# Optimization experiments

Hardware: AMD Instinct MI355X
Metric: run time of the kernel (lower is better)

Reference implementation:

```python
import jax, jax.numpy as jnp
import numpy as np
from jax import lax

GROUPS = 32


def _fps(xyz, m):
    # farthest point sampling; indices are non-differentiable selections
    xyz = lax.stop_gradient(xyz)
    B, N, _ = xyz.shape

    def step(carry, _):
        dist, far = carry
        c = jnp.take_along_axis(xyz, far[:, None, None], axis=1)  # [B,1,3]
        d = jnp.sum((xyz - c) ** 2, axis=-1)                       # [B,N]
        dist = jnp.minimum(dist, d)
        return (dist, jnp.argmax(dist, axis=1)), far

    init = (jnp.full((B, N), 1e10, xyz.dtype), jnp.zeros((B,), jnp.int32))
    _, cent = lax.scan(step, init, None, length=m)
    return jnp.transpose(cent)  # [B,m]


def _sqdist(a, b):
    # [B,Na,3] x [B,Nb,3] -> [B,Na,Nb]
    return (jnp.sum(a * a, -1)[:, :, None] + jnp.sum(b * b, -1)[:, None, :]
            - 2.0 * jnp.einsum('bnc,bmc->bnm', a, b))


def _gather(feat, idx):
    # feat [B,S,C], idx [B,N,k] -> [B,N,k,C]
    return jax.vmap(lambda f, i: f[i])(feat, idx)


def _edge_conv(f, idx, W, b):
    nbr = _gather(f, idx)                                # [B,S,k,C]
    ctr = jnp.broadcast_to(f[:, :, None, :], nbr.shape)
    e = jnp.concatenate([ctr, nbr - ctr], axis=-1)       # [B,S,k,2C]
    h = jax.nn.relu(jnp.einsum('bske,ec->bskc', e, W) + b)
    return jnp.max(h, axis=2)                            # [B,S,C']


def _graph_encoder(x, k, layers, Wo, bo):
    d2 = _sqdist(x[..., :3], x[..., :3])
    idx = lax.top_k(-d2, k)[1]                           # kNN on coords (incl. self)
    f = x
    for W, b in layers:
        f = _edge_conv(f, idx, W, b)
    return f @ Wo + bo


def _upsample(fs, xd, xs):
    # 3-NN inverse-distance interpolation, matches torch.cdist/topk path
    d = jnp.sqrt(jnp.maximum(_sqdist(xd, xs), 0.0))      # euclidean like cdist
    negv, idx = lax.top_k(-d, 3)
    w = 1.0 / (-negv + 1e-8)
    w = w / jnp.sum(w, -1, keepdims=True)
    fk = _gather(fs, idx)                                # [B,Nd,3,C]
    return jnp.sum(fk * w[..., None], axis=2)


def _group_norm(x, g, b):
    B, N, C = x.shape
    xg = x.reshape(B, N, GROUPS, C // GROUPS)
    mu = xg.mean(-1, keepdims=True)
    var = xg.var(-1, keepdims=True)
    xn = ((xg - mu) * lax.rsqrt(var + 1e-5)).reshape(B, N, C)
    return xn * g + b


def _pos_encoding(N, d):
    pos = jnp.arange(N, dtype=jnp.float32)[:, None]
    div = jnp.exp(jnp.arange(0, d, 2, dtype=jnp.float32) * (-np.log(10000.0) / d))
    ang = pos * div
    return jnp.stack([jnp.sin(ang), jnp.cos(ang)], axis=-1).reshape(N, d)


def _forward(x,
             e1_W0, e1_b0, e1_W1, e1_b1, e1_Wo, e1_bo,
             e2_W0, e2_b0, e2_W1, e2_b1, e2_Wo, e2_bo,
             e3_W0, e3_b0, e3_W1, e3_b1, e3_W2, e3_b2, e3_Wo, e3_bo,
             f_W1, f_b1, g1_w, g1_b, f_W2, f_b2, g2_w, g2_b):
    B, N, C = x.shape
    encs = [
        (512, 16, [(e1_W0, e1_b0), (e1_W1, e1_b1)], e1_Wo, e1_bo),
        (1024, 32, [(e2_W0, e2_b0), (e2_W1, e2_b1)], e2_Wo, e2_bo),
        (2048, 64, [(e3_W0, e3_b0), (e3_W1, e3_b1), (e3_W2, e3_b2)], e3_Wo, e3_bo),
    ]
    feats = []
    for scale, k, layers, Wo, bo in encs:
        if N > scale:
            idx = _fps(x[..., :3], scale)
            xs = jnp.take_along_axis(x, idx[:, :, None], axis=1)  # [B,scale,C]
        else:
            xs = x
        f = _graph_encoder(xs, k, layers, Wo, bo)
        if f.shape[1] < N:
            f = _upsample(f, x[..., :3], xs[..., :3])
        feats.append(f)
    fused = jnp.concatenate(feats, axis=-1)               # [B,N,1280]
    h = jax.nn.relu(_group_norm(fused @ f_W1 + f_b1, g1_w, g1_b))
    h = jax.nn.relu(_group_norm(h @ f_W2 + f_b2, g2_w, g2_b))
    return h + _pos_encoding(N, h.shape[-1])[None]


def setup_inputs() -> dict:
    key = jax.random.key(0)
    ks = iter(jax.random.split(key, 64))

    def W(shape, s=0.05):
        return jax.random.normal(next(ks), shape, jnp.float32) * s

    inp = {"x": jax.random.normal(next(ks), (2, 4096, 6), jnp.float32)}
    # encoder 1: in 6, hidden [128,256], out 256, k=16
    inp.update(e1_W0=W((12, 128)), e1_b0=jnp.zeros(128), e1_W1=W((256, 256)), e1_b1=jnp.zeros(256),
               e1_Wo=W((256, 256)), e1_bo=jnp.zeros(256))
    # encoder 2: in 6, hidden [256,512], out 512, k=32
    inp.update(e2_W0=W((12, 256)), e2_b0=jnp.zeros(256), e2_W1=W((512, 512)), e2_b1=jnp.zeros(512),
               e2_Wo=W((512, 512)), e2_bo=jnp.zeros(512))
    # encoder 3: in 6, hidden [128,256,512], out 512, k=64
    inp.update(e3_W0=W((12, 128)), e3_b0=jnp.zeros(128), e3_W1=W((256, 256)), e3_b1=jnp.zeros(256),
               e3_W2=W((512, 512)), e3_b2=jnp.zeros(512), e3_Wo=W((512, 512)), e3_bo=jnp.zeros(512))
    # fusion: 1280 -> 512 -> 512 with GroupNorm(32, 512)
    inp.update(f_W1=W((1280, 512)), f_b1=jnp.zeros(512), g1_w=jnp.ones(512), g1_b=jnp.zeros(512),
               f_W2=W((512, 512)), f_b2=jnp.zeros(512), g2_w=jnp.ones(512), g2_b=jnp.zeros(512))
    return inp


def reference(x,
              e1_W0, e1_b0, e1_W1, e1_b1, e1_Wo, e1_bo,
              e2_W0, e2_b0, e2_W1, e2_b1, e2_Wo, e2_bo,
              e3_W0, e3_b0, e3_W1, e3_b1, e3_W2, e3_b2, e3_Wo, e3_bo,
              f_W1, f_b1, g1_w, g1_b, f_W2, f_b2, g2_w, g2_b):
    return _forward(x,
                    e1_W0, e1_b0, e1_W1, e1_b1, e1_Wo, e1_bo,
                    e2_W0, e2_b0, e2_W1, e2_b1, e2_Wo, e2_bo,
                    e3_W0, e3_b0, e3_W1, e3_b1, e3_W2, e3_b2, e3_Wo, e3_bo,
                    f_W1, f_b1, g1_w, g1_b, f_W2, f_b2, g2_w, g2_b)
```

## Files before the change

### kernel.cpp

```cpp
#include <hip/hip_runtime.h>
#include <math.h>

#define OFF_CENT   0x0
#define OFF_XSP    0x20000
#define OFF_XS6    0x40000
#define OFF_KNN    0x60000
#define OFF_F      0x180000
#define OFF_UV     0xA00000
#define OFF_G      0x1A00000
#define OFF_WCAT   0x2200000
#define OFF_BCAT   0x2400000
#define OFF_FUSED  0x2500000
#define OFF_T      0x180000
#define OFF_H1     0x1200000
#define OFF_T2     0x2200000

__device__ __forceinline__ unsigned fkey_flip(float f) {
  unsigned u = __float_as_uint(f);
  return u ^ ((u >> 31) ? 0xFFFFFFFFu : 0x80000000u);
}
__device__ __forceinline__ float fkey_unflip(unsigned k) {
  unsigned u = k ^ ((k >> 31) ? 0x80000000u : 0xFFFFFFFFu);
  return __uint_as_float(u);
}

template<int CTRL>
__device__ __forceinline__ float dpp_max_stepf(float v) {
  int t = __builtin_amdgcn_update_dpp(__float_as_int(v), __float_as_int(v),
                                      CTRL, 0xf, 0xf, false);
  return fmaxf(v, __int_as_float(t));
}
__device__ __forceinline__ float wave64_max(float v) {
  v = dpp_max_stepf<0x111>(v);
  v = dpp_max_stepf<0x112>(v);
  v = dpp_max_stepf<0x114>(v);
  v = dpp_max_stepf<0x118>(v);
  v = dpp_max_stepf<0x142>(v);
  v = dpp_max_stepf<0x143>(v);
  return __int_as_float(__builtin_amdgcn_readlane(__float_as_int(v), 63));
}
__device__ __forceinline__ unsigned long long u64max(unsigned long long a,
                                                    unsigned long long b) {
  return a > b ? a : b;
}

__global__ __launch_bounds__(512) void fps_kernel(const float* __restrict__ x,
                                                  int* __restrict__ cent)
{
  int b = blockIdx.x, tid = threadIdx.x;
  __shared__ float4 C4[4096];
  __shared__ __align__(16) unsigned long long slots[2][8];
  float px[8], py[8], pz[8], dist[8];
#pragma unroll
  for (int i = 0; i < 8; ++i) {
    int p = tid + 512 * i;
    const float* r = x + ((long)b * 4096 + p) * 6;
    px[i] = r[0]; py[i] = r[1]; pz[i] = r[2];
    C4[p] = make_float4(px[i], py[i], pz[i], 0.0f);
    dist[i] = 1e10f;
  }
  if (tid == 0) cent[b * 2048] = 0;
  __syncthreads();
  float4 c0 = C4[0];
  float cx = c0.x, cy = c0.y, cz = c0.z;
  int wid = tid >> 6, lane = tid & 63;
  for (int j = 1; j < 2048; ++j) {
    float m = -1.0f;
#pragma unroll
    for (int i = 0; i < 8; ++i) {
      float dx = __fsub_rn(px[i], cx);
      float dy = __fsub_rn(py[i], cy);
      float dz = __fsub_rn(pz[i], cz);
      float d  = __fadd_rn(__fadd_rn(__fmul_rn(dx,dx), __fmul_rn(dy,dy)), __fmul_rn(dz,dz));
      float nd = fminf(dist[i], d);
      dist[i] = nd;
      m = fmaxf(m, nd);
    }
    float wm = wave64_max(m);
    unsigned long long mm = 0ULL; unsigned ii = 0;
#pragma unroll
    for (int i = 7; i >= 0; --i) {
      unsigned long long mi = __ballot(dist[i] == wm);
      if (mi) { mm = mi; ii = (unsigned)i; }
    }
    int lane_w = __ffsll((unsigned long long)mm) - 1;
    unsigned idx_w = (unsigned)(wid * 64 + lane_w) + 512u * ii;
    if (lane == 0)
      slots[j & 1][wid] = ((unsigned long long)__float_as_uint(wm) << 32)
                        | (unsigned)(0xFFFFFFFFu - idx_w);
    __syncthreads();
    const unsigned long long* sl = slots[j & 1];
    ulonglong2 sA = *(const ulonglong2*)&sl[0];
    ulonglong2 sB = *(const ulonglong2*)&sl[2];
    ulonglong2 sC = *(const ulonglong2*)&sl[4];
    ulonglong2 sD = *(const ulonglong2*)&sl[6];
    unsigned long long kk = u64max(u64max(u64max(sA.x, sA.y), u64max(sB.x, sB.y)),
                                   u64max(u64max(sC.x, sC.y), u64max(sD.x, sD.y)));
    unsigned idx = 0xFFFFFFFFu - (unsigned)kk;
    float4 c = C4[idx];
    cx = c.x; cy = c.y; cz = c.z;
    if (tid == 0) cent[b * 2048 + j] = idx;
  }
}

__global__ void gather_xs_kernel(const float* __restrict__ x, const int* __restrict__ cent,
                                 float* __restrict__ xs6, float4* __restrict__ xsp)
{
  int t = blockIdx.x * 256 + threadIdx.x;
  if (t >= 2 * 2048) return;
  int b = t >> 11;
  int p = cent[t];
  const float* src = x + ((long)b * 4096 + p) * 6;
  float* dst = xs6 + (long)t * 6;
#pragma unroll
  for (int c = 0; c < 6; ++c) dst[c] = src[c];
  xsp[t] = make_float4(src[0], src[1], src[2], 0.0f);
}

template<int S, int K>
__global__ __launch_bounds__(256) void knn_kernel(const float4* __restrict__ xsp,
                                                  int* __restrict__ out)
{
  constexpr int NI = S / 64;
  __shared__ float4 P[S];
  int b = (blockIdx.x * 4) / S;
  int wid = threadIdx.x >> 6, lane = threadIdx.x & 63;
  int s = (blockIdx.x * 4 + wid) & (S - 1);
  for (int i = threadIdx.x; i < S; i += 256) P[i] = xsp[b * 2048 + i];
  __syncthreads();
  float4 Q = P[s];
  float saq = __fadd_rn(__fadd_rn(__fmul_rn(Q.x,Q.x), __fmul_rn(Q.y,Q.y)), __fmul_rn(Q.z,Q.z));
  float dd[NI];
#pragma unroll
  for (int i = 0; i < NI; ++i) {
    float4 c = P[i * 64 + lane];
    float sac = __fadd_rn(__fadd_rn(__fmul_rn(c.x,c.x), __fmul_rn(c.y,c.y)), __fmul_rn(c.z,c.z));
    float dot = __fadd_rn(__fadd_rn(__fmul_rn(Q.x,c.x), __fmul_rn(Q.y,c.y)), __fmul_rn(Q.z,c.z));
    dd[i] = __fsub_rn(__fadd_rn(saq, sac), __fmul_rn(2.0f, dot));
  }
  long obase = ((long)b * S + s) * K;
  for (int t = 0; t < K; ++t) {
    float bv = INFINITY; int bi = 0;
#pragma unroll
    for (int i = 0; i < NI; ++i) if (dd[i] < bv) { bv = dd[i]; bi = i; }
    unsigned long long key = ((unsigned long long)fkey_flip(bv) << 32)
                           | (unsigned)(bi * 64 + lane);
#pragma unroll
    for (int m = 32; m; m >>= 1) {
      unsigned long long o = __shfl_xor(key, m, 64);
      if (o < key) key = o;
    }
    unsigned cand = (unsigned)key;
    if ((int)(cand & 63) == lane) {
      int slot = cand >> 6;
#pragma unroll
      for (int i = 0; i < NI; ++i) if (i == slot) dd[i] = INFINITY;
    }
    if (lane == 0) out[obase + t] = (int)cand;
  }
}

__global__ void wcat_prep(const float* __restrict__ W, const float* __restrict__ bias,
                          int C, int Cp, float* __restrict__ Wcat, float* __restrict__ bcat)
{
  int n2 = 2 * Cp;
  int total = C * n2;
  for (int t = blockIdx.x * 256 + threadIdx.x; t < total + n2; t += gridDim.x * 256) {
    if (t < total) {
      int c = t / n2, n = t % n2;
      Wcat[t] = (n < Cp) ? (W[c * Cp + n] - W[(C + c) * Cp + n]) : W[(C + c) * Cp + (n - Cp)];
    } else {
      int n = t - total;
      bcat[n] = (n < Cp) ? bias[n] : 0.0f;
    }
  }
}

__global__ __launch_bounds__(256) void gemm_bias(
    const float* __restrict__ A, long strideA, int lda,
    const float* __restrict__ W, int N, int K,
    const float* __restrict__ bias,
    float* __restrict__ C, long strideC, int ldc)
{
  A += (long)blockIdx.z * strideA;
  C += (long)blockIdx.z * strideC;
  int rowBase = blockIdx.x * 64, colBase = blockIdx.y * 64;
  __shared__ float As[16][68];
  __shared__ float Ws[16][68];
  int tid = threadIdx.x;
  int tx = tid & 15, ty = tid >> 4;
  float acc[4][4] = {};
  for (int k0 = 0; k0 < K; k0 += 16) {
    {
      int r = tid >> 2, c0 = (tid & 3) * 4;
      const float* Ar = A + (long)(rowBase + r) * lda + k0 + c0;
#pragma unroll
      for (int u = 0; u < 4; ++u) {
        float val = 0.0f;
        if (k0 + c0 + u < K) val = Ar[u];
        As[c0 + u][r] = val;
      }
    }
    {
      int c = tid & 63, kr = tid >> 6;
#pragma unroll
      for (int u = 0; u < 4; ++u) {
        int kk = kr + u * 4;
        float val = 0.0f;
        if (k0 + kk < K) val = W[(long)(k0 + kk) * N + colBase + c];
        Ws[kk][c] = val;
      }
    }
    __syncthreads();
#pragma unroll
    for (int kk = 0; kk < 16; ++kk) {
      float4 av = *(const float4*)&As[kk][ty * 4];
      float4 wv = *(const float4*)&Ws[kk][tx * 4];
      float a_[4] = {av.x, av.y, av.z, av.w};
      float w_[4] = {wv.x, wv.y, wv.z, wv.w};
#pragma unroll
      for (int i = 0; i < 4; ++i)
#pragma unroll
        for (int j = 0; j < 4; ++j)
          acc[i][j] = fmaf(a_[i], w_[j], acc[i][j]);
    }
    __syncthreads();
  }
#pragma unroll
  for (int i = 0; i < 4; ++i) {
    int r = rowBase + ty * 4 + i;
    int c0 = colBase + tx * 4;
    float4 o;
    o.x = acc[i][0] + bias[c0 + 0];
    o.y = acc[i][1] + bias[c0 + 1];
    o.z = acc[i][2] + bias[c0 + 2];
    o.w = acc[i][3] + bias[c0 + 3];
    *(float4*)&C[(long)r * ldc + c0] = o;
  }
}

__global__ __launch_bounds__(256) void gemm_bias_big(
    const float* __restrict__ A, int lda,
    const float* __restrict__ W, int N, int K,
    const float* __restrict__ bias,
    float* __restrict__ C, int ldc)
{
  int rowBase = blockIdx.x * 128, colBase = blockIdx.y * 128;
  __shared__ float As[16][132];
  __shared__ float Ws[16][132];
  int tid = threadIdx.x;
  int tx = tid & 15, ty = tid >> 4;
  float acc[8][8] = {};
  for (int k0 = 0; k0 < K; k0 += 16) {
    {
      int r = tid >> 1, c0 = (tid & 1) * 8;
      const float* Ar = A + (long)(rowBase + r) * lda + k0 + c0;
      float4 v0 = *(const float4*)(Ar);
      float4 v1 = *(const float4*)(Ar + 4);
      As[c0 + 0][r] = v0.x; As[c0 + 1][r] = v0.y; As[c0 + 2][r] = v0.z; As[c0 + 3][r] = v0.w;
      As[c0 + 4][r] = v1.x; As[c0 + 5][r] = v1.y; As[c0 + 6][r] = v1.z; As[c0 + 7][r] = v1.w;
    }
    {
      int kr = tid >> 4, c0 = (tid & 15) * 8;
      const float* Wr = W + (long)(k0 + kr) * N + colBase + c0;
      float4 w0 = *(const float4*)(Wr);
      float4 w1 = *(const float4*)(Wr + 4);
      *(float4*)&Ws[kr][c0]     = w0;
      *(float4*)&Ws[kr][c0 + 4] = w1;
    }
    __syncthreads();
#pragma unroll
    for (int kk = 0; kk < 16; ++kk) {
      float a_[8], w_[8];
      *(float4*)&a_[0] = *(const float4*)&As[kk][ty * 8];
      *(float4*)&a_[4] = *(const float4*)&As[kk][ty * 8 + 4];
      *(float4*)&w_[0] = *(const float4*)&Ws[kk][tx * 8];
      *(float4*)&w_[4] = *(const float4*)&Ws[kk][tx * 8 + 4];
#pragma unroll
      for (int i = 0; i < 8; ++i)
#pragma unroll
        for (int jj = 0; jj < 8; ++jj)
          acc[i][jj] = fmaf(a_[i], w_[jj], acc[i][jj]);
    }
    __syncthreads();
  }
#pragma unroll
  for (int i = 0; i < 8; ++i) {
    int r = rowBase + ty * 8 + i;
    int c0 = colBase + tx * 8;
    float4 o0, o1;
    o0.x = acc[i][0] + bias[c0 + 0];
    o0.y = acc[i][1] + bias[c0 + 1];
    o0.z = acc[i][2] + bias[c0 + 2];
    o0.w = acc[i][3] + bias[c0 + 3];
    o1.x = acc[i][4] + bias[c0 + 4];
    o1.y = acc[i][5] + bias[c0 + 5];
    o1.z = acc[i][6] + bias[c0 + 6];
    o1.w = acc[i][7] + bias[c0 + 7];
    *(float4*)&C[(long)r * ldc + c0]     = o0;
    *(float4*)&C[(long)r * ldc + c0 + 4] = o1;
  }
}

__global__ void edge_agg(const float* __restrict__ UV, const int* __restrict__ idx,
                         int S, int k, int Cp, float* __restrict__ F)
{
  int bs = blockIdx.x;
  int b = bs / S;
  __shared__ int nb[64];
  if ((int)threadIdx.x < k) nb[threadIdx.x] = idx[(long)bs * k + threadIdx.x];
  __syncthreads();
  int ld = 2 * Cp;
  const float* Ub = UV + (long)bs * ld;
  for (int c = threadIdx.x; c < Cp; c += blockDim.x) {
    float m = -INFINITY;
    for (int j = 0; j < k; ++j) {
      float v = UV[(long)(b * S + nb[j]) * ld + Cp + c];
      m = fmaxf(m, v);
    }
    float r = Ub[c] + m;
    F[(long)bs * Cp + c] = r > 0.0f ? r : 0.0f;
  }
}

template<int S, int CP>
__global__ __launch_bounds__(256) void upsample_kernel(
    const float* __restrict__ x, const float4* __restrict__ xsp,
    const float* __restrict__ G, float* __restrict__ fused, int colOff)
{
  constexpr int NI = S / 64;
  __shared__ float4 P[S];
  int b = (blockIdx.x * 4) >> 12;
  int wid = threadIdx.x >> 6, lane = threadIdx.x & 63;
  int n = (blockIdx.x * 4 + wid) & 4095;
  for (int i = threadIdx.x; i < S; i += 256) P[i] = xsp[b * 2048 + i];
  __syncthreads();
  const float* q = x + ((long)b * 4096 + n) * 6;
  float qx = q[0], qy = q[1], qz = q[2];
  float saq = __fadd_rn(__fadd_rn(__fmul_rn(qx,qx), __fmul_rn(qy,qy)), __fmul_rn(qz,qz));
  float dd[NI];
#pragma unroll
  for (int i = 0; i < NI; ++i) {
    float4 c = P[i * 64 + lane];
    float sac = __fadd_rn(__fadd_rn(__fmul_rn(c.x,c.x), __fmul_rn(c.y,c.y)), __fmul_rn(c.z,c.z));
    float dot = __fadd_rn(__fadd_rn(__fmul_rn(qx,c.x), __fmul_rn(qy,c.y)), __fmul_rn(qz,c.z));
    dd[i] = __fsub_rn(__fadd_rn(saq, sac), __fmul_rn(2.0f, dot));
  }
  int id[3]; float w[3];
  for (int t = 0; t < 3; ++t) {
    float bv = INFINITY; int bi = 0;
#pragma unroll
    for (int i = 0; i < NI; ++i) if (dd[i] < bv) { bv = dd[i]; bi = i; }
    unsigned long long key = ((unsigned long long)fkey_flip(bv) << 32)
                           | (unsigned)(bi * 64 + lane);
#pragma unroll
    for (int m = 32; m; m >>= 1) {
      unsigned long long o = __shfl_xor(key, m, 64);
      if (o < key) key = o;
    }
    unsigned cand = (unsigned)key;
    float d2 = fkey_unflip((unsigned)(key >> 32));
    float d = __fsqrt_rn(fmaxf(d2, 0.0f));
    id[t] = (int)cand;
    w[t] = 1.0f / __fadd_rn(d, 1e-8f);
    if ((int)(cand & 63) == lane) {
      int slot = cand >> 6;
#pragma unroll
      for (int i = 0; i < NI; ++i) if (i == slot) dd[i] = INFINITY;
    }
  }
  float wsum = __fadd_rn(__fadd_rn(w[0], w[1]), w[2]);
  float w0 = w[0] / wsum, w1 = w[1] / wsum, w2 = w[2] / wsum;
  const float* g0 = G + (long)(b * S + id[0]) * CP;
  const float* g1 = G + (long)(b * S + id[1]) * CP;
  const float* g2 = G + (long)(b * S + id[2]) * CP;
  float* orow = fused + ((long)b * 4096 + n) * 1280 + colOff;
#pragma unroll
  for (int t = 0; t < CP / 64; ++t) {
    int c = lane + 64 * t;
    float v = __fadd_rn(__fadd_rn(__fmul_rn(w0, g0[c]), __fmul_rn(w1, g1[c])),
                        __fmul_rn(w2, g2[c]));
    orow[c] = v;
  }
}

__global__ __launch_bounds__(256) void gn_kernel(const float* __restrict__ T,
    const float* __restrict__ gw, const float* __restrict__ gb,
    float* __restrict__ out, int addPos)
{
  int t = blockIdx.x * 256 + threadIdx.x;
  int row = t >> 5, g = t & 31;
  const float* p = T + (long)row * 512 + g * 16;
  float v[16];
#pragma unroll
  for (int i = 0; i < 4; ++i) {
    float4 f = *(const float4*)(p + i * 4);
    v[i*4+0] = f.x; v[i*4+1] = f.y; v[i*4+2] = f.z; v[i*4+3] = f.w;
  }
  float s = 0.0f;
#pragma unroll
  for (int i = 0; i < 16; ++i) s += v[i];
  float mu = s * 0.0625f;
  float var = 0.0f;
#pragma unroll
  for (int i = 0; i < 16; ++i) { float d = v[i] - mu; var += d * d; }
  var *= 0.0625f;
  float inv = 1.0f / sqrtf(var + 1e-5f);
  int cbase = g * 16;
  int n = row & 4095;
  float o[16];
#pragma unroll
  for (int i = 0; i < 16; ++i) {
    int c = cbase + i;
    float y = (v[i] - mu) * inv * gw[c] + gb[c];
    y = y > 0.0f ? y : 0.0f;
    if (addPos) {
      int half = c >> 1;
      float div = expf((float)(2 * half) * -0.017988946039016358f);
      float ang = (float)n * div;
      y += (c & 1) ? cosf(ang) : sinf(ang);
    }
    o[i] = y;
  }
  float* d = out + (long)row * 512 + cbase;
#pragma unroll
  for (int i = 0; i < 4; ++i) {
    float4 f; f.x = o[i*4+0]; f.y = o[i*4+1]; f.z = o[i*4+2]; f.w = o[i*4+3];
    *(float4*)(d + i * 4) = f;
  }
}

static inline void launch_gemm(const float* A, long strideA, int lda,
                               const float* W, const float* bias,
                               float* C, long strideC, int ldc,
                               int Mb, int N, int K, int nb, hipStream_t s)
{
  dim3 grid(Mb / 64, N / 64, nb);
  gemm_bias<<<grid, 256, 0, s>>>(A, strideA, lda, W, N, K, bias, C, strideC, ldc);
}
static inline void launch_gemm_big(const float* A, int lda,
                                   const float* W, const float* bias,
                                   float* C, int ldc,
                                   int M, int N, int K, hipStream_t s)
{
  dim3 grid(M / 128, N / 128, 1);
  gemm_bias_big<<<grid, 256, 0, s>>>(A, lda, W, N, K, bias, C, ldc);
}

extern "C" void kernel_launch(void* const* d_in, const int* in_sizes, int n_in,
                              void* d_out, int out_size, void* d_ws, size_t ws_size,
                              hipStream_t stream)
{
  const float* x     = (const float*)d_in[0];
  const float* e1_W0 = (const float*)d_in[1];  const float* e1_b0 = (const float*)d_in[2];
  const float* e1_W1 = (const float*)d_in[3];  const float* e1_b1 = (const float*)d_in[4];
  const float* e1_Wo = (const float*)d_in[5];  const float* e1_bo = (const float*)d_in[6];
  const float* e2_W0 = (const float*)d_in[7];  const float* e2_b0 = (const float*)d_in[8];
  const float* e2_W1 = (const float*)d_in[9];  const float* e2_b1 = (const float*)d_in[10];
  const float* e2_Wo = (const float*)d_in[11]; const float* e2_bo = (const float*)d_in[12];
  const float* e3_W0 = (const float*)d_in[13]; const float* e3_b0 = (const float*)d_in[14];
  const float* e3_W1 = (const float*)d_in[15]; const float* e3_b1 = (const float*)d_in[16];
  const float* e3_W2 = (const float*)d_in[17]; const float* e3_b2 = (const float*)d_in[18];
  const float* e3_Wo = (const float*)d_in[19]; const float* e3_bo = (const float*)d_in[20];
  const float* f_W1  = (const float*)d_in[21]; const float* f_b1  = (const float*)d_in[22];
  const float* g1_w  = (const float*)d_in[23]; const float* g1_b  = (const float*)d_in[24];
  const float* f_W2  = (const float*)d_in[25]; const float* f_b2  = (const float*)d_in[26];
  const float* g2_w  = (const float*)d_in[27]; const float* g2_b  = (const float*)d_in[28];

  char* ws = (char*)d_ws;
  int*    cent  = (int*)(ws + OFF_CENT);
  float4* xsp   = (float4*)(ws + OFF_XSP);
  float*  xs6   = (float*)(ws + OFF_XS6);
  int*    knn   = (int*)(ws + OFF_KNN);
  float*  F     = (float*)(ws + OFF_F);
  float*  UV    = (float*)(ws + OFF_UV);
  float*  G     = (float*)(ws + OFF_G);
  float*  WCAT  = (float*)(ws + OFF_WCAT);
  float*  BCAT  = (float*)(ws + OFF_BCAT);
  float*  FUSED = (float*)(ws + OFF_FUSED);
  float*  T     = (float*)(ws + OFF_T);
  float*  H1    = (float*)(ws + OFF_H1);
  float*  T2    = (float*)(ws + OFF_T2);

  fps_kernel<<<2, 512, 0, stream>>>(x, cent);
  gather_xs_kernel<<<16, 256, 0, stream>>>(x, cent, xs6, xsp);

  knn_kernel<512,16><<<256, 256, 0, stream>>>(xsp, knn);
  wcat_prep<<<256, 256, 0, stream>>>(e1_W0, e1_b0, 6, 128, WCAT, BCAT);
  launch_gemm(xs6, (long)2048*6, 6, WCAT, BCAT, UV, (long)512*256, 256, 512, 256, 6, 2, stream);
  edge_agg<<<dim3(2*512), 128, 0, stream>>>(UV, knn, 512, 16, 128, F);
  wcat_prep<<<256, 256, 0, stream>>>(e1_W1, e1_b1, 128, 256, WCAT, BCAT);
  launch_gemm(F, 0, 128, WCAT, BCAT, UV, 0, 512, 1024, 512, 128, 1, stream);
  edge_agg<<<dim3(2*512), 256, 0, stream>>>(UV, knn, 512, 16, 256, F);
  launch_gemm(F, 0, 256, e1_Wo, e1_bo, G, 0, 256, 1024, 256, 256, 1, stream);
  upsample_kernel<512,256><<<2048, 256, 0, stream>>>(x, xsp, G, FUSED, 0);

  knn_kernel<1024,32><<<512, 256, 0, stream>>>(xsp, knn);
  wcat_prep<<<256, 256, 0, stream>>>(e2_W0, e2_b0, 6, 256, WCAT, BCAT);
  launch_gemm(xs6, (long)2048*6, 6, WCAT, BCAT, UV, (long)1024*512, 512, 1024, 512, 6, 2, stream);
  edge_agg<<<dim3(2*1024), 256, 0, stream>>>(UV, knn, 1024, 32, 256, F);
  wcat_prep<<<256, 256, 0, stream>>>(e2_W1, e2_b1, 256, 512, WCAT, BCAT);
  launch_gemm_big(F, 256, WCAT, BCAT, UV, 1024, 2048, 1024, 256, stream);
  edge_agg<<<dim3(2*1024), 256, 0, stream>>>(UV, knn, 1024, 32, 512, F);
  launch_gemm(F, 0, 512, e2_Wo, e2_bo, G, 0, 512, 2048, 512, 512, 1, stream);
  upsample_kernel<1024,512><<<2048, 256, 0, stream>>>(x, xsp, G, FUSED, 256);

  knn_kernel<2048,64><<<1024, 256, 0, stream>>>(xsp, knn);
  wcat_prep<<<256, 256, 0, stream>>>(e3_W0, e3_b0, 6, 128, WCAT, BCAT);
  launch_gemm(xs6, (long)2048*6, 6, WCAT, BCAT, UV, (long)2048*256, 256, 2048, 256, 6, 2, stream);
  edge_agg<<<dim3(2*2048), 128, 0, stream>>>(UV, knn, 2048, 64, 128, F);
  wcat_prep<<<256, 256, 0, stream>>>(e3_W1, e3_b1, 128, 256, WCAT, BCAT);
  launch_gemm_big(F, 128, WCAT, BCAT, UV, 512, 4096, 512, 128, stream);
  edge_agg<<<dim3(2*2048), 256, 0, stream>>>(UV, knn, 2048, 64, 256, F);
  wcat_prep<<<256, 256, 0, stream>>>(e3_W2, e3_b2, 256, 512, WCAT, BCAT);
  launch_gemm_big(F, 256, WCAT, BCAT, UV, 1024, 4096, 1024, 256, stream);
  edge_agg<<<dim3(2*2048), 256, 0, stream>>>(UV, knn, 2048, 64, 512, F);
  launch_gemm_big(F, 512, e3_Wo, e3_bo, G, 512, 4096, 512, 512, stream);
  upsample_kernel<2048,512><<<2048, 256, 0, stream>>>(x, xsp, G, FUSED, 768);

  launch_gemm_big(FUSED, 1280, f_W1, f_b1, T, 512, 8192, 512, 1280, stream);
  gn_kernel<<<1024, 256, 0, stream>>>(T, g1_w, g1_b, H1, 0);
  launch_gemm_big(H1, 512, f_W2, f_b2, T2, 512, 8192, 512, 512, stream);
  gn_kernel<<<1024, 256, 0, stream>>>(T2, g2_w, g2_b, (float*)d_out, 1);
}
```

Baseline: 2.309 ms.

## Sort FPS points by Morton cell and skip chunks via bounding-box pruning

The farthest-point-sampling kernel now bins points into an 8x8x8 Morton grid, sorts them into spatially coherent 64-point chunks and stores a per-chunk bounding box. Each iteration updates distances only for chunks whose box could lie closer to the new centroid than their current max, keeping a per-chunk best value and index. This is meant to avoid the full 4096-point distance update on every one of the 2048 serial steps, at the cost of extra setup, divergence and tie-breaking bookkeeping. The edge aggregation and upsample kernels are also vectorised to float4 loads and stores, with edge_agg launched with Cp/4 threads.

After: 3.945 ms. +70.9%, slower.

```diff
diff --git a/kernel.cpp b/kernel.cpp
--- a/kernel.cpp
+++ b/kernel.cpp
@@ -39,55 +39,201 @@
   v = dpp_max_stepf<0x143>(v);
   return __int_as_float(__builtin_amdgcn_readlane(__float_as_int(v), 63));
 }
+template<int CTRL>
+__device__ __forceinline__ float dpp_min_stepf(float v) {
+  int t = __builtin_amdgcn_update_dpp(__float_as_int(v), __float_as_int(v),
+                                      CTRL, 0xf, 0xf, false);
+  return fminf(v, __int_as_float(t));
+}
+__device__ __forceinline__ float wave64_min(float v) {
+  v = dpp_min_stepf<0x111>(v);
+  v = dpp_min_stepf<0x112>(v);
+  v = dpp_min_stepf<0x114>(v);
+  v = dpp_min_stepf<0x118>(v);
+  v = dpp_min_stepf<0x142>(v);
+  v = dpp_min_stepf<0x143>(v);
+  return __int_as_float(__builtin_amdgcn_readlane(__float_as_int(v), 63));
+}
+template<int CTRL>
+__device__ __forceinline__ unsigned dpp_min_stepu(unsigned v) {
+  unsigned t = (unsigned)__builtin_amdgcn_update_dpp((int)v, (int)v,
+                                                     CTRL, 0xf, 0xf, false);
+  return v < t ? v : t;
+}
+__device__ __forceinline__ unsigned wave64_min_u32(unsigned v) {
+  v = dpp_min_stepu<0x111>(v);
+  v = dpp_min_stepu<0x112>(v);
+  v = dpp_min_stepu<0x114>(v);
+  v = dpp_min_stepu<0x118>(v);
+  v = dpp_min_stepu<0x142>(v);
+  v = dpp_min_stepu<0x143>(v);
+  return (unsigned)__builtin_amdgcn_readlane((int)v, 63);
+}
 __device__ __forceinline__ unsigned long long u64max(unsigned long long a,
                                                     unsigned long long b) {
   return a > b ? a : b;
 }
+__device__ __forceinline__ unsigned spread3(unsigned v) {
+  return (v & 1u) | ((v & 2u) << 2) | ((v & 4u) << 4);
+}
 
 __global__ __launch_bounds__(512) void fps_kernel(const float* __restrict__ x,
                                                   int* __restrict__ cent)
 {
   int b = blockIdx.x, tid = threadIdx.x;
-  __shared__ float4 C4[4096];
+  int wid = tid >> 6, lane = tid & 63;
+  __shared__ float4 ss4[4096];
+  __shared__ float bb[64 * 6];
+  __shared__ unsigned hist[512];
+  __shared__ unsigned sc[512];
+  __shared__ unsigned bbm[6];
   __shared__ __align__(16) unsigned long long slots[2][8];
+
   float px[8], py[8], pz[8], dist[8];
+  unsigned spk[8];
 #pragma unroll
   for (int i = 0; i < 8; ++i) {
     int p = tid + 512 * i;
     const float* r = x + ((long)b * 4096 + p) * 6;
     px[i] = r[0]; py[i] = r[1]; pz[i] = r[2];
-    C4[p] = make_float4(px[i], py[i], pz[i], 0.0f);
+  }
+  if (tid < 6) bbm[tid] = (tid < 3) ? 0xFFFFFFFFu : 0u;
+  if (tid < 512) hist[tid] = 0u;
+  if (tid == 0) cent[b * 2048] = 0;
+  __syncthreads();
+
+  {
+    float lx = px[0], hx = px[0], ly = py[0], hy = py[0], lz = pz[0], hz = pz[0];
+#pragma unroll
+    for (int i = 1; i < 8; ++i) {
+      lx = fminf(lx, px[i]); hx = fmaxf(hx, px[i]);
+      ly = fminf(ly, py[i]); hy = fmaxf(hy, py[i]);
+      lz = fminf(lz, pz[i]); hz = fmaxf(hz, pz[i]);
+    }
+    lx = wave64_min(lx); hx = wave64_max(hx);
+    ly = wave64_min(ly); hy = wave64_max(hy);
+    lz = wave64_min(lz); hz = wave64_max(hz);
+    if (lane == 0) {
+      atomicMin(&bbm[0], fkey_flip(lx)); atomicMax(&bbm[3], fkey_flip(hx));
+      atomicMin(&bbm[1], fkey_flip(ly)); atomicMax(&bbm[4], fkey_flip(hy));
+      atomicMin(&bbm[2], fkey_flip(lz)); atomicMax(&bbm[5], fkey_flip(hz));
+    }
+  }
+  __syncthreads();
+  float lox = fkey_unflip(bbm[0]), loy = fkey_unflip(bbm[1]), loz = fkey_unflip(bbm[2]);
+  float hix = fkey_unflip(bbm[3]), hiy = fkey_unflip(bbm[4]), hiz = fkey_unflip(bbm[5]);
+  float sxf = (hix > lox) ? 8.0f / (hix - lox) : 0.0f;
+  float syf = (hiy > loy) ? 8.0f / (hiy - loy) : 0.0f;
+  float szf = (hiz > loz) ? 8.0f / (hiz - loz) : 0.0f;
+
+#pragma unroll
+  for (int i = 0; i < 8; ++i) {
+    int ix = min(7, max(0, (int)((px[i] - lox) * sxf)));
+    int iy = min(7, max(0, (int)((py[i] - loy) * syf)));
+    int iz = min(7, max(0, (int)((pz[i] - loz) * szf)));
+    unsigned cell = spread3((unsigned)ix) | (spread3((unsigned)iy) << 1)
+                  | (spread3((unsigned)iz) << 2);
+    atomicAdd(&hist[cell], 1u);
+  }
+  __syncthreads();
+
+  unsigned myc = hist[tid];
+  unsigned run = myc;
+  for (int s = 1; s < 512; s <<= 1) {
+    sc[tid] = run;
+    __syncthreads();
+    if (tid >= s) run += sc[tid - s];
+    __syncthreads();
+  }
+  hist[tid] = run - myc;
+  __syncthreads();
+
+#pragma unroll
+  for (int i = 0; i < 8; ++i) {
+    int ix = min(7, max(0, (int)((px[i] - lox) * sxf)));
+    int iy = min(7, max(0, (int)((py[i] - loy) * syf)));
+    int iz = min(7, max(0, (int)((pz[i] - loz) * szf)));
+    unsigned cell = spread3((unsigned)ix) | (spread3((unsigned)iy) << 1)
+                  | (spread3((unsigned)iz) << 2);
+    unsigned pos = atomicAdd(&hist[cell], 1u);
+    ss4[pos] = make_float4(px[i], py[i], pz[i],
+                           __uint_as_float((unsigned)(tid + 512 * i)));
+  }
+  __syncthreads();
+
+#pragma unroll
+  for (int i = 0; i < 8; ++i) {
+    int pos = wid * 512 + i * 64 + lane;
+    float4 c = ss4[pos];
+    px[i] = c.x; py[i] = c.y; pz[i] = c.z;
+    unsigned oidx = __float_as_uint(c.w);
+    spk[i] = (oidx << 12) | (unsigned)pos;
     dist[i] = 1e10f;
   }
-  if (tid == 0) cent[b * 2048] = 0;
-  __syncthreads();
-  float4 c0 = C4[0];
-  float cx = c0.x, cy = c0.y, cz = c0.z;
-  int wid = tid >> 6, lane = tid & 63;
+
+#pragma unroll
+  for (int i = 0; i < 8; ++i) {
+    float lx = wave64_min(px[i]), hx = wave64_max(px[i]);
+    float ly = wave64_min(py[i]), hy = wave64_max(py[i]);
+    float lz = wave64_min(pz[i]), hz = wave64_max(pz[i]);
+    if (lane == 0) {
+      float* bp = &bb[(wid * 8 + i) * 6];
+      bp[0] = lx; bp[1] = hx; bp[2] = ly; bp[3] = hy; bp[4] = lz; bp[5] = hz;
+    }
+  }
+  float candval = 1e10f;
+  unsigned candpk = 0;
+#pragma unroll
+  for (int i = 0; i < 8; ++i) {
+    unsigned im = wave64_min_u32(spk[i]);
+    if (lane == i) candpk = im;
+  }
+  float blox = 0, bhxx = 0, bloy = 0, bhxy = 0, bloz = 0, bhxz = 0;
+  __syncthreads();
+  if (lane < 8) {
+    const float* bp = &bb[(wid * 8 + lane) * 6];
+    blox = bp[0]; bhxx = bp[1]; bloy = bp[2]; bhxy = bp[3]; bloz = bp[4]; bhxz = bp[5];
+  }
+
+  const float* r0 = x + (long)b * 4096 * 6;
+  float cx = r0[0], cy = r0[1], cz = r0[2];
+
   for (int j = 1; j < 2048; ++j) {
-    float m = -1.0f;
-#pragma unroll
-    for (int i = 0; i < 8; ++i) {
-      float dx = __fsub_rn(px[i], cx);
-      float dy = __fsub_rn(py[i], cy);
-      float dz = __fsub_rn(pz[i], cz);
-      float d  = __fadd_rn(__fadd_rn(__fmul_rn(dx,dx), __fmul_rn(dy,dy)), __fmul_rn(dz,dz));
-      float nd = fminf(dist[i], d);
-      dist[i] = nd;
-      m = fmaxf(m, nd);
-    }
-    float wm = wave64_max(m);
-    unsigned long long mm = 0ULL; unsigned ii = 0;
-#pragma unroll
-    for (int i = 7; i >= 0; --i) {
-      unsigned long long mi = __ballot(dist[i] == wm);
-      if (mi) { mm = mi; ii = (unsigned)i; }
-    }
-    int lane_w = __ffsll((unsigned long long)mm) - 1;
-    unsigned idx_w = (unsigned)(wid * 64 + lane_w) + 512u * ii;
-    if (lane == 0)
-      slots[j & 1][wid] = ((unsigned long long)__float_as_uint(wm) << 32)
-                        | (unsigned)(0xFFFFFFFFu - idx_w);
+    float dxm = fmaxf(fmaxf(blox - cx, cx - bhxx), 0.0f);
+    float dym = fmaxf(fmaxf(bloy - cy, cy - bhxy), 0.0f);
+    float dzm = fmaxf(fmaxf(bloz - cz, cz - bhxz), 0.0f);
+    float md2 = dxm * dxm + dym * dym + dzm * dzm;
+    bool upd = (lane < 8) && (md2 * 0.99999f < candval);
+    unsigned long long umask = __ballot(upd) & 0xFFull;
+    if (umask) {
+#pragma unroll
+      for (int i = 0; i < 8; ++i) {
+        if (umask & (1ull << i)) {
+          float dx = __fsub_rn(px[i], cx);
+          float dy = __fsub_rn(py[i], cy);
+          float dz = __fsub_rn(pz[i], cz);
+          float d  = __fadd_rn(__fadd_rn(__fmul_rn(dx, dx), __fmul_rn(dy, dy)),
+                               __fmul_rn(dz, dz));
+          float nd = fminf(dist[i], d);
+          dist[i] = nd;
+          float vm = wave64_max(nd);
+          unsigned mi = (nd == vm) ? spk[i] : 0xFFFFFFFFu;
+          unsigned im = wave64_min_u32(mi);
+          if (lane == i) { candval = vm; candpk = im; }
+        }
+      }
+    }
+    unsigned long long best = 0ULL;
+#pragma unroll
+    for (int l = 0; l < 8; ++l) {
+      unsigned vb = (unsigned)__builtin_amdgcn_readlane(__float_as_int(candval), l);
+      unsigned pk = (unsigned)__builtin_amdgcn_readlane((int)candpk, l);
+      unsigned long long key = ((unsigned long long)vb << 24)
+                             | (unsigned long long)(((~(pk >> 12)) & 0xFFFu) << 12)
+                             | (unsigned long long)(pk & 0xFFFu);
+      best = u64max(best, key);
+    }
+    if (lane == 0) slots[j & 1][wid] = best;
     __syncthreads();
     const unsigned long long* sl = slots[j & 1];
     ulonglong2 sA = *(const ulonglong2*)&sl[0];
@@ -96,10 +242,11 @@
     ulonglong2 sD = *(const ulonglong2*)&sl[6];
     unsigned long long kk = u64max(u64max(u64max(sA.x, sA.y), u64max(sB.x, sB.y)),
                                    u64max(u64max(sC.x, sC.y), u64max(sD.x, sD.y)));
-    unsigned idx = 0xFFFFFFFFu - (unsigned)kk;
-    float4 c = C4[idx];
+    unsigned pos  = (unsigned)(kk & 0xFFFu);
+    unsigned oidx = (~((unsigned)(kk >> 12))) & 0xFFFu;
+    float4 c = ss4[pos];
     cx = c.x; cy = c.y; cz = c.z;
-    if (tid == 0) cent[b * 2048 + j] = idx;
+    if (tid == 0) cent[b * 2048 + j] = (int)oidx;
   }
 }
 
@@ -311,15 +458,23 @@
   if ((int)threadIdx.x < k) nb[threadIdx.x] = idx[(long)bs * k + threadIdx.x];
   __syncthreads();
   int ld = 2 * Cp;
-  const float* Ub = UV + (long)bs * ld;
-  for (int c = threadIdx.x; c < Cp; c += blockDim.x) {
-    float m = -INFINITY;
+  int nf4 = Cp >> 2;
+  for (int c4 = threadIdx.x; c4 < nf4; c4 += blockDim.x) {
+    float4 m = make_float4(-INFINITY, -INFINITY, -INFINITY, -INFINITY);
     for (int j = 0; j < k; ++j) {
-      float v = UV[(long)(b * S + nb[j]) * ld + Cp + c];
-      m = fmaxf(m, v);
-    }
-    float r = Ub[c] + m;
-    F[(long)bs * Cp + c] = r > 0.0f ? r : 0.0f;
+      const float4* vp = (const float4*)(UV + (long)(b * S + nb[j]) * ld + Cp);
+      float4 v = vp[c4];
+      m.x = fmaxf(m.x, v.x); m.y = fmaxf(m.y, v.y);
+      m.z = fmaxf(m.z, v.z); m.w = fmaxf(m.w, v.w);
+    }
+    float4 u = ((const float4*)(UV + (long)bs * ld))[c4];
+    float4 o;
+    o.x = u.x + m.x; o.y = u.y + m.y; o.z = u.z + m.z; o.w = u.w + m.w;
+    o.x = o.x > 0.0f ? o.x : 0.0f;
+    o.y = o.y > 0.0f ? o.y : 0.0f;
+    o.z = o.z > 0.0f ? o.z : 0.0f;
+    o.w = o.w > 0.0f ? o.w : 0.0f;
+    ((float4*)(F + (long)bs * Cp))[c4] = o;
   }
 }
 
@@ -371,16 +526,20 @@
   }
   float wsum = __fadd_rn(__fadd_rn(w[0], w[1]), w[2]);
   float w0 = w[0] / wsum, w1 = w[1] / wsum, w2 = w[2] / wsum;
-  const float* g0 = G + (long)(b * S + id[0]) * CP;
-  const float* g1 = G + (long)(b * S + id[1]) * CP;
-  const float* g2 = G + (long)(b * S + id[2]) * CP;
-  float* orow = fused + ((long)b * 4096 + n) * 1280 + colOff;
-#pragma unroll
-  for (int t = 0; t < CP / 64; ++t) {
-    int c = lane + 64 * t;
-    float v = __fadd_rn(__fadd_rn(__fmul_rn(w0, g0[c]), __fmul_rn(w1, g1[c])),
-                        __fmul_rn(w2, g2[c]));
-    orow[c] = v;
+  const float4* g0 = (const float4*)(G + (long)(b * S + id[0]) * CP);
+  const float4* g1 = (const float4*)(G + (long)(b * S + id[1]) * CP);
+  const float4* g2 = (const float4*)(G + (long)(b * S + id[2]) * CP);
+  float4* orow = (float4*)(fused + ((long)b * 4096 + n) * 1280 + colOff);
+#pragma unroll
+  for (int t = 0; t < CP / 256; ++t) {
+    int c4 = lane + 64 * t;
+    float4 a = g0[c4], bb4 = g1[c4], cc = g2[c4];
+    float4 v;
+    v.x = __fadd_rn(__fadd_rn(__fmul_rn(w0, a.x), __fmul_rn(w1, bb4.x)), __fmul_rn(w2, cc.x));
+    v.y = __fadd_rn(__fadd_rn(__fmul_rn(w0, a.y), __fmul_rn(w1, bb4.y)), __fmul_rn(w2, cc.y));
+    v.z = __fadd_rn(__fadd_rn(__fmul_rn(w0, a.z), __fmul_rn(w1, bb4.z)), __fmul_rn(w2, cc.z));
+    v.w = __fadd_rn(__fadd_rn(__fmul_rn(w0, a.w), __fmul_rn(w1, bb4.w)), __fmul_rn(w2, cc.w));
+    orow[c4] = v;
   }
 }
 
@@ -445,6 +604,12 @@
 {
   dim3 grid(M / 128, N / 128, 1);
   gemm_bias_big<<<grid, 256, 0, s>>>(A, lda, W, N, K, bias, C, ldc);
+}
+static inline void launch_edge(const float* UV, const int* knn, int S, int k, int Cp,
+                               float* F, hipStream_t s)
+{
+  int threads = Cp / 4 < 64 ? 64 : Cp / 4;
+  edge_agg<<<dim3(2 * S), threads, 0, s>>>(UV, knn, S, k, Cp, F);
 }
 
 extern "C" void kernel_launch(void* const* d_in, const int* in_sizes, int n_in,
@@ -488,33 +653,33 @@
   knn_kernel<512,16><<<256, 256, 0, stream>>>(xsp, knn);
   wcat_prep<<<256, 256, 0, stream>>>(e1_W0, e1_b0, 6, 128, WCAT, BCAT);
   launch_gemm(xs6, (long)2048*6, 6, WCAT, BCAT, UV, (long)512*256, 256, 512, 256, 6, 2, stream);
-  edge_agg<<<dim3(2*512), 128, 0, stream>>>(UV, knn, 512, 16, 128, F);
+  launch_edge(UV, knn, 512, 16, 128, F, stream);
   wcat_prep<<<256, 256, 0, stream>>>(e1_W1, e1_b1, 128, 256, WCAT, BCAT);
   launch_gemm(F, 0, 128, WCAT, BCAT, UV, 0, 512, 1024, 512, 128, 1, stream);
-  edge_agg<<<dim3(2*512), 256, 0, stream>>>(UV, knn, 512, 16, 256, F);
+  launch_edge(UV, knn, 512, 16, 256, F, stream);
   launch_gemm(F, 0, 256, e1_Wo, e1_bo, G, 0, 256, 1024, 256, 256, 1, stream);
   upsample_kernel<512,256><<<2048, 256, 0, stream>>>(x, xsp, G, FUSED, 0);
 
   knn_kernel<1024,32><<<512, 256, 0, stream>>>(xsp, knn);
   wcat_prep<<<256, 256, 0, stream>>>(e2_W0, e2_b0, 6, 256, WCAT, BCAT);
   launch_gemm(xs6, (long)2048*6, 6, WCAT, BCAT, UV, (long)1024*512, 512, 1024, 512, 6, 2, stream);
-  edge_agg<<<dim3(2*1024), 256, 0, stream>>>(UV, knn, 1024, 32, 256, F);
+  launch_edge(UV, knn, 1024, 32, 256, F, stream);
   wcat_prep<<<256, 256, 0, stream>>>(e2_W1, e2_b1, 256, 512, WCAT, BCAT);
   launch_gemm_big(F, 256, WCAT, BCAT, UV, 1024, 2048, 1024, 256, stream);
-  edge_agg<<<dim3(2*1024), 256, 0, stream>>>(UV, knn, 1024, 32, 512, F);
+  launch_edge(UV, knn, 1024, 32, 512, F, stream);
   launch_gemm(F, 0, 512, e2_Wo, e2_bo, G, 0, 512, 2048, 512, 512, 1, stream);
   upsample_kernel<1024,512><<<2048, 256, 0, stream>>>(x, xsp, G, FUSED, 256);
 
   knn_kernel<2048,64><<<1024, 256, 0, stream>>>(xsp, knn);
   wcat_prep<<<256, 256, 0, stream>>>(e3_W0, e3_b0, 6, 128, WCAT, BCAT);
   launch_gemm(xs6, (long)2048*6, 6, WCAT, BCAT, UV, (long)2048*256, 256, 2048, 256, 6, 2, stream);
-  edge_agg<<<dim3(2*2048), 128, 0, stream>>>(UV, knn, 2048, 64, 128, F);
+  launch_edge(UV, knn, 2048, 64, 128, F, stream);
   wcat_prep<<<256, 256, 0, stream>>>(e3_W1, e3_b1, 128, 256, WCAT, BCAT);
   launch_gemm_big(F, 128, WCAT, BCAT, UV, 512, 4096, 512, 128, stream);
-  edge_agg<<<dim3(2*2048), 256, 0, stream>>>(UV, knn, 2048, 64, 256, F);
+  launch_edge(UV, knn, 2048, 64, 256, F, stream);
   wcat_prep<<<256, 256, 0, stream>>>(e3_W2, e3_b2, 256, 512, WCAT, BCAT);
   launch_gemm_big(F, 256, WCAT, BCAT, UV, 1024, 4096, 1024, 256, stream);
-  edge_agg<<<dim3(2*2048), 256, 0, stream>>>(UV, knn, 2048, 64, 512, F);
+  launch_edge(UV, knn, 2048, 64, 512, F, stream);
   launch_gemm_big(F, 512, e3_Wo, e3_bo, G, 512, 4096, 512, 512, stream);
   upsample_kernel<2048,512><<<2048, 256, 0, stream>>>(x, xsp, G, FUSED, 768);
 
```
